# Kernel optimization log

Hardware: AMD Instinct MI355X
Metric: run time of the kernel (lower is better)

The kernel has to match this reference:

```python
import jax, jax.numpy as jnp
import numpy as np

B = 64            # graphs in batch
N = 100_000       # total nodes
E = 600_000       # total edges of g == nodes of line graph lg
E2 = 1_500_000    # edges of line graph
H = 128           # hidden_dim
L = 3             # num_layers
MAXZ = 100

seg_sum = jax.ops.segment_sum


def setup_inputs() -> dict:
    key = jax.random.key(0)
    ks = jax.random.split(key, 20)
    s = 1.0 / np.sqrt(H)
    inp = {
        'z': jax.random.randint(ks[0], (N,), 0, MAXZ + 1),
        'd': jax.random.uniform(ks[1], (E, 1), dtype=jnp.float32),
        'src': jax.random.randint(ks[2], (E,), 0, N),
        'dst': jax.random.randint(ks[3], (E,), 0, N),
        'lsrc': jax.random.randint(ks[4], (E2,), 0, E),
        'ldst': jax.random.randint(ks[5], (E2,), 0, E),
        'node_graph': jnp.sort(jax.random.randint(ks[6], (N,), 0, B)),
        'edge_graph': jnp.sort(jax.random.randint(ks[7], (E,), 0, B)),
        'emb': jax.random.normal(ks[8], (MAXZ + 1, H), jnp.float32),
        'ep_w': jax.random.normal(ks[9], (1, H), jnp.float32) * s,
        'ep_b': jnp.zeros((H,), jnp.float32),
        'gW': jax.random.normal(ks[10], (L, H, H), jnp.float32) * s,
        'gb': jnp.zeros((L, H), jnp.float32),
        'lgW': jax.random.normal(ks[11], (L, H, H), jnp.float32) * s,
        'lgb': jnp.zeros((L, H), jnp.float32),
        'r1w': jax.random.normal(ks[12], (2 * H, H), jnp.float32) * s,
        'r1b': jnp.zeros((H,), jnp.float32),
        'r2w': jax.random.normal(ks[13], (H, 1), jnp.float32) * s,
        'r2b': jnp.zeros((1,), jnp.float32),
    }
    return inp


def _graph_conv(h, srcix, dstix, W, b, n_nodes):
    # DGL GraphConv, norm='both', aggregate-then-weight (in==out dims):
    # h' = D_in^{-1/2} * A^T * (D_out^{-1/2} * h) @ W + b, degrees clamped >= 1
    ones = jnp.ones(srcix.shape[0], h.dtype)
    deg_out = jnp.clip(seg_sum(ones, srcix, num_segments=n_nodes), 1.0)
    deg_in = jnp.clip(seg_sum(ones, dstix, num_segments=n_nodes), 1.0)
    m = h * (deg_out ** -0.5)[:, None]
    agg = seg_sum(m[srcix], dstix, num_segments=n_nodes)  # SpMM gather-scatter
    agg = agg * (deg_in ** -0.5)[:, None]
    return agg @ W + b


def _segment_mean(h, seg, n_seg):
    sums = seg_sum(h, seg, num_segments=n_seg)
    cnt = jnp.clip(seg_sum(jnp.ones(h.shape[0], h.dtype), seg, num_segments=n_seg), 1.0)
    return sums / cnt[:, None]


def reference(z, d, src, dst, lsrc, ldst, node_graph, edge_graph,
              emb, ep_w, ep_b, gW, gb, lgW, lgb, r1w, r1b, r2w, r2b):
    h = emb[z]                       # [N, H]
    e = d @ ep_w + ep_b              # [E, H]
    for i in range(L):
        h = jax.nn.relu(_graph_conv(h, src, dst, gW[i], gb[i], N))
    for i in range(L):
        e = jax.nn.relu(_graph_conv(e, lsrc, ldst, lgW[i], lgb[i], E))
    hg = _segment_mean(h, node_graph, B)   # [B, H]
    he = _segment_mean(e, edge_graph, B)   # [B, H]
    x = jnp.concatenate([hg, he], axis=-1)  # [B, 2H]
    y = jax.nn.silu(x @ r1w + r1b) @ r2w + r2b
    return y.reshape(-1)             # [B]
```

## Files before the change

### kernel.cpp

```cpp
#include <hip/hip_runtime.h>
#include <math.h>

#define H 128
typedef unsigned short u16;
typedef unsigned char u8;
typedef unsigned int u32;
typedef _Float16 f16;
typedef f16 f16x8 __attribute__((ext_vector_type(8)));
typedef float f32x4 __attribute__((ext_vector_type(4)));
typedef float f32x2 __attribute__((ext_vector_type(2)));

#if __has_builtin(__builtin_amdgcn_cvt_pk_fp8_f32)
#define HW8 1
#else
#define HW8 0
#endif

#define SSTRIDE 144

static inline int cdiv(long long a, long long b) { return (int)((a + b - 1) / b); }

__device__ __forceinline__ int swz_seg(int orig, int n) {
    int q = n >> 3, r = n & 7;
    int x = orig & 7;
    int base = (x < r) ? x * (q + 1) : r * (q + 1) + (x - r) * q;
    return base + (orig >> 3);
}
__device__ __forceinline__ int conv_bid(int orig, int nbCN, int nwg) {
    return (orig < nbCN) ? swz_seg(orig, nbCN)
                         : nbCN + swz_seg(orig - nbCN, nwg - nbCN);
}

struct F8 {
    static __device__ inline float dec(u8 v) {
        int e = (v >> 3) & 15, m = v & 7;
        float f = (e == 0) ? (float)m * 0.001953125f : ldexpf(1.f + 0.125f * (float)m, e - 7);
        return (v & 0x80) ? -f : f;
    }
    static __device__ inline u8 enc(float x) {
        u8 s = (u8)((__float_as_uint(x) >> 24) & 0x80);
        float ax = fabsf(x);
        if (!(ax < 448.f)) return s | 0x7E;
        if (ax < 0.015625f) {
            int m = (int)rintf(ax * 512.f);
            if (m >= 8) return s | 0x08;
            return s | (u8)m;
        }
        int e; float fr = frexpf(ax, &e);
        int E = e - 1;
        int m = (int)rintf(fr * 16.f - 8.f);
        if (m == 8) { m = 0; ++E; }
        if (E > 8) return s | 0x7E;
        return s | (u8)(((E + 7) << 3) | m);
    }
};

static __device__ inline u32 enc4(float x0, float x1, float x2, float x3) {
#if HW8
    u32 w = __builtin_amdgcn_cvt_pk_fp8_f32(x0, x1, 0, false);
    w = __builtin_amdgcn_cvt_pk_fp8_f32(x2, x3, w, true);
    return w;
#else
    union { u8 b[4]; u32 u; } p;
    p.b[0] = F8::enc(x0); p.b[1] = F8::enc(x1); p.b[2] = F8::enc(x2); p.b[3] = F8::enc(x3);
    return p.u;
#endif
}
static __device__ inline float4 dec4(u32 v) {
#if HW8
    f32x2 lo = __builtin_amdgcn_cvt_pk_f32_fp8(v, false);
    f32x2 hi = __builtin_amdgcn_cvt_pk_f32_fp8(v, true);
    return make_float4(lo.x, lo.y, hi.x, hi.y);
#else
    union { u32 u; u8 b[4]; } c; c.u = v;
    return make_float4(F8::dec(c.b[0]), F8::dec(c.b[1]), F8::dec(c.b[2]), F8::dec(c.b[3]));
#endif
}

__global__ __launch_bounds__(256) void setup1_k(
    const float* __restrict__ gW, const float* __restrict__ lgW, f16* __restrict__ wt, int L, int nbPW,
    const int* __restrict__ src, const int* __restrict__ dst,
    const int* __restrict__ lsrc, const int* __restrict__ ldst,
    int* __restrict__ con, int* __restrict__ cin, int* __restrict__ coe, int* __restrict__ cie,
    int E, int E2, int nbHI,
    const int* __restrict__ node_graph, int N, const int* __restrict__ edge_graph,
    int B, int* __restrict__ cntn, int* __restrict__ cnte,
    const float* __restrict__ epw, const float* __restrict__ epb, float* __restrict__ uv) {
    int blk = blockIdx.x;
    if (blk < nbPW) {
        int mat = blk >> 6;
        int idx = (blk & 63) * 256 + threadIdx.x;
        int k = idx >> 7, n = idx & 127;
        const float* W = (mat < L) ? gW + (size_t)mat * H * H : lgW + (size_t)(mat - L) * H * H;
        wt[(size_t)mat * H * H + (size_t)n * H + k] = (f16)W[(size_t)k * H + n];
        return;
    }
    blk -= nbPW;
    if (blk < nbHI) {
        int i = blk * 256 + threadIdx.x;
        if (i < E) {
            atomicAdd(&con[src[i]], 1);
            atomicAdd(&cin[dst[i]], 1);
        } else if (i < E + E2) {
            int j = i - E;
            atomicAdd(&coe[lsrc[j]], 1);
            atomicAdd(&cie[ldst[j]], 1);
        }
        return;
    }
    blk -= nbHI;
    if (blk < 2) {
        const int* seg = blk ? edge_graph : node_graph;
        int n = blk ? E : N;
        int* cnt = blk ? cnte : cntn;
        __shared__ int bound[129];
        int b = threadIdx.x;
        if (b <= B) {
            int lo = 0, hi = n;
            while (lo < hi) {
                int mid = (lo + hi) >> 1;
                if (seg[mid] < b) lo = mid + 1; else hi = mid;
            }
            bound[b] = lo;
        }
        __syncthreads();
        if (b < B) cnt[b] = bound[b + 1] - bound[b];
        return;
    }
    {
        int n = threadIdx.x;
        if (n < H) {
            float su = 0.f, sv = 0.f;
            for (int k = 0; k < H; ++k) {
                float w = lgW[(size_t)k * H + n];
                su = fmaf(epw[k], w, su);
                sv = fmaf(epb[k], w, sv);
            }
            uv[n] = su;
            uv[n + H] = sv;
        }
    }
}

__global__ __launch_bounds__(256) void setup2_k(
    const int* __restrict__ con, const int* __restrict__ cin,
    const int* __restrict__ coe, const int* __restrict__ cie,
    float* __restrict__ ron, float* __restrict__ rin,
    float* __restrict__ roe, float* __restrict__ rie,
    const float* __restrict__ d, float2* __restrict__ pairE, int N, int E, int nbRS,
    int* __restrict__ offs_n, int nbN, int* __restrict__ offs_e, int* __restrict__ bsum) {
    int blk = blockIdx.x;
    if (blk < nbRS) {
        int i = blk * 256 + threadIdx.x;
        if (i < N) { int v = con[i]; ron[i] = rsqrtf((float)(v < 1 ? 1 : v)); }
        else if (i < 2 * N) { int n = i - N; int v = cin[n]; rin[n] = rsqrtf((float)(v < 1 ? 1 : v)); }
        else if (i < 2 * N + E) {
            int n = i - 2 * N; int v = coe[n];
            float r = rsqrtf((float)(v < 1 ? 1 : v));
            roe[n] = r;
            pairE[n] = make_float2(r * d[n], r);
        } else if (i < 2 * N + 2 * E) {
            int n = i - 2 * N - E; int v = cie[n]; rie[n] = rsqrtf((float)(v < 1 ? 1 : v));
        }
        return;
    }
    blk -= nbRS;
    {
        __shared__ int sh[256];
        const int* in; int* out; int n; int gid;
        if (blk < nbN) { in = cin; out = offs_n; n = N; gid = blk * 256 + threadIdx.x; }
        else { in = cie; out = offs_e; n = E; gid = (blk - nbN) * 256 + threadIdx.x; }
        int v = (gid < n) ? in[gid] : 0;
        sh[threadIdx.x] = v;
        __syncthreads();
        for (int off = 1; off < 256; off <<= 1) {
            int t = (threadIdx.x >= off) ? sh[threadIdx.x - off] : 0;
            __syncthreads();
            sh[threadIdx.x] += t;
            __syncthreads();
        }
        if (gid < n) out[gid] = sh[threadIdx.x] - v;
        if (threadIdx.x == 255) bsum[blk] = sh[255];
    }
}

__global__ __launch_bounds__(256) void scan_bsum2_k(int* __restrict__ bsum, int nbA, int nbB) {
    __shared__ int sh[256];
    __shared__ int carry;
#pragma unroll 1
    for (int part = 0; part < 2; ++part) {
        int base0 = part ? nbA : 0;
        int nb = part ? nbB : nbA;
        if (threadIdx.x == 0) carry = 0;
        __syncthreads();
        for (int base = 0; base < nb; base += 256) {
            int i = base + threadIdx.x;
            int v = (i < nb) ? bsum[base0 + i] : 0;
            sh[threadIdx.x] = v;
            __syncthreads();
            for (int off = 1; off < 256; off <<= 1) {
                int t = (threadIdx.x >= off) ? sh[threadIdx.x - off] : 0;
                __syncthreads();
                sh[threadIdx.x] += t;
                __syncthreads();
            }
            if (i < nb) bsum[base0 + i] = sh[threadIdx.x] - v + carry;
            __syncthreads();
            if (threadIdx.x == 0) carry += sh[255];
            __syncthreads();
        }
    }
}

__global__ __launch_bounds__(256) void setup3_k(
    int* __restrict__ offs_n, int* __restrict__ cur_n, int N, int nbN, int E,
    int* __restrict__ offs_e, int* __restrict__ cur_e, int E2, int nbE,
    const int* __restrict__ bsum,
    const int* __restrict__ z, const float* __restrict__ emb,
    const float* __restrict__ ron, u8* __restrict__ featN) {
    int blk = blockIdx.x;
    int nbSA = nbN + nbE;
    if (blk < nbSA) {
        int* offs; int* curp; int n; int gid; int nnz;
        if (blk < nbN) { offs = offs_n; curp = cur_n; n = N; gid = blk * 256 + threadIdx.x; nnz = E; }
        else { offs = offs_e; curp = cur_e; n = E; gid = (blk - nbN) * 256 + threadIdx.x; nnz = E2; }
        if (gid < n) {
            int v = offs[gid] + bsum[blk];
            offs[gid] = v;
            curp[gid] = v;
        }
        if (gid == 0) offs[n] = nnz;
        return;
    }
    blk -= nbSA;
    {
        int idx = blk * 256 + threadIdx.x;
        if (idx >= N * 32) return;
        int n = idx >> 5, c4 = (idx & 31) << 2;
        float sc = ron[n];
        const float4 v = *(const float4*)(emb + (size_t)z[n] * H + c4);
        *(u32*)(featN + (size_t)n * H + c4) = enc4(v.x * sc, v.y * sc, v.z * sc, v.w * sc);
    }
}

__global__ __launch_bounds__(256) void fill2_k(const int* __restrict__ src, const int* __restrict__ dst,
                                               const int* __restrict__ lsrc, const int* __restrict__ ldst,
                                               int* __restrict__ cur_n, int* __restrict__ cur_e,
                                               uint2* __restrict__ nbr_n, uint2* __restrict__ nbr_e,
                                               const float2* __restrict__ pairE, float2* __restrict__ pslot,
                                               int E, int E2) {
    int i = blockIdx.x * 256 + threadIdx.x;
    if (i < E) {
        int dd = dst[i];
        int p = atomicAdd(&cur_n[dd], 1);
        nbr_n[p] = make_uint2((u32)src[i], (u32)dd);
    } else if (i < E + E2) {
        int j = i - E;
        int ls = lsrc[j];
        int dd = ldst[j];
        int p = atomicAdd(&cur_e[dd], 1);
        nbr_e[p] = make_uint2((u32)ls, (u32)dd);
        pslot[p] = pairE[ls];
    }
}

__device__ __forceinline__ void gather_phase(
    const u8* __restrict__ Xin,
    const int* __restrict__ offs, const uint2* __restrict__ nbr2,
    const float* __restrict__ rs_in, int M,
    int row0, f16 (*As)[136], int wave, int lane) {
    const int rowbase = row0 + wave * 16;
    {
        uint2* zp = (uint2*)&As[wave * 16][0];
#pragma unroll
        for (int i = 0; i < 9; ++i) {
            int o = lane + i * 64;
            if (o < 544) zp[o] = make_uint2(0u, 0u);
        }
    }
    const int gl = lane >> 4;
    const int ln = lane & 15;
    const int rbase4 = rowbase + gl * 4;
    const int r_lo = min(rbase4, M);
    const int r_hi = min(rbase4 + 4, M);
    const int jbeg = offs[r_lo];
    const int jend = offs[r_hi];
    if (jbeg >= jend) return;
    const int mrow = M - 1;
    const float rsr0 = rs_in[min(rbase4 + 0, mrow)];
    const float rsr1 = rs_in[min(rbase4 + 1, mrow)];
    const float rsr2 = rs_in[min(rbase4 + 2, mrow)];
    const float rsr3 = rs_in[min(rbase4 + 3, mrow)];

    float a0 = 0.f, a1 = 0.f, a2 = 0.f, a3 = 0.f, a4 = 0.f, a5 = 0.f, a6 = 0.f, a7 = 0.f;
    int curdst = -1;

#define FLUSH_ROW()                                                              \
    do {                                                                         \
        const int dd_ = curdst - rbase4;                                         \
        const float ri_ = dd_ == 0 ? rsr0 : (dd_ == 1 ? rsr1 : (dd_ == 2 ? rsr2 : rsr3)); \
        f16x8 o_;                                                                \
        o_[0] = (f16)(a0 * ri_); o_[1] = (f16)(a1 * ri_);                        \
        o_[2] = (f16)(a2 * ri_); o_[3] = (f16)(a3 * ri_);                        \
        o_[4] = (f16)(a4 * ri_); o_[5] = (f16)(a5 * ri_);                        \
        o_[6] = (f16)(a6 * ri_); o_[7] = (f16)(a7 * ri_);                        \
        *(f16x8*)&As[curdst - row0][ln << 3] = o_;                               \
    } while (0)

#define PROC_BATCH(eX, fX)                                                       \
    _Pragma("unroll")                                                            \
    for (int k = 0; k < 8; ++k) {                                                \
        if (jc + k < jend) {                                                     \
            const int dk = (int)eX[k].y;                                         \
            if (dk != curdst) {                                                  \
                if (curdst >= 0) {                                               \
                    FLUSH_ROW();                                                 \
                    a0 = a1 = a2 = a3 = a4 = a5 = a6 = a7 = 0.f;                 \
                }                                                                \
                curdst = dk;                                                     \
            }                                                                    \
            float4 lo = dec4(fX[k].x);                                           \
            float4 hi = dec4(fX[k].y);                                           \
            a0 += lo.x; a1 += lo.y; a2 += lo.z; a3 += lo.w;                      \
            a4 += hi.x; a5 += hi.y; a6 += hi.z; a7 += hi.w;                      \
        }                                                                        \
    }

    uint2 eA[8], eB[8], fA[8], fB[8];
#pragma unroll
    for (int k = 0; k < 8; ++k) eA[k] = nbr2[min(jbeg + k, jend - 1)];
#pragma unroll
    for (int k = 0; k < 8; ++k) eB[k] = nbr2[min(jbeg + 8 + k, jend - 1)];
#pragma unroll
    for (int k = 0; k < 8; ++k)
        fA[k] = *(const uint2*)(Xin + ((size_t)eA[k].x << 7) + (ln << 3));
    int jc = jbeg;
    for (;;) {
        if (jc + 8 < jend) {
#pragma unroll
            for (int k = 0; k < 8; ++k)
                fB[k] = *(const uint2*)(Xin + ((size_t)eB[k].x << 7) + (ln << 3));
        }
        __builtin_amdgcn_sched_barrier(0);
        PROC_BATCH(eA, fA);
        if (jc + 16 < jend) {
#pragma unroll
            for (int k = 0; k < 8; ++k) eA[k] = nbr2[min(jc + 16 + k, jend - 1)];
        }
        jc += 8;
        if (jc >= jend) break;
        if (jc + 8 < jend) {
#pragma unroll
            for (int k = 0; k < 8; ++k)
                fA[k] = *(const uint2*)(Xin + ((size_t)eA[k].x << 7) + (ln << 3));
        }
        __builtin_amdgcn_sched_barrier(0);
        PROC_BATCH(eB, fB);
        if (jc + 16 < jend) {
#pragma unroll
            for (int k = 0; k < 8; ++k) eB[k] = nbr2[min(jc + 16 + k, jend - 1)];
        }
        jc += 8;
        if (jc >= jend) break;
    }
    FLUSH_ROW();
#undef PROC_BATCH
#undef FLUSH_ROW
}

template <bool STORE>
__device__ __forceinline__ void conv_mfma_phase(
    u8* __restrict__ Xout, const f16* __restrict__ Wt, const float* __restrict__ bias,
    const float* __restrict__ scale_out, int M, int row0, f16 (*As)[136], int wave, int lane) {
    const int rowbase = row0 + wave * 16;
    if (rowbase >= M) return;
    const int l15 = lane & 15;
    const int quad = lane >> 4;

    f16x8 a[4];
#pragma unroll
    for (int kt = 0; kt < 4; ++kt)
        a[kt] = *(const f16x8*)&As[wave * 16 + l15][kt * 32 + quad * 8];

    float rsc[4];
#pragma unroll
    for (int r = 0; r < 4; ++r) {
        int gr = rowbase + quad * 4 + r;
        rsc[r] = (scale_out && gr < M) ? scale_out[gr] : 1.f;
    }

    u8* stage = (u8*)&As[wave * 16][0];

#pragma unroll
    for (int n0 = 0; n0 < 8; ++n0) {
        f32x4 acc = {0.f, 0.f, 0.f, 0.f};
        const f16* bp = Wt + (size_t)(n0 * 16 + l15) * H + quad * 8;
#pragma unroll
        for (int kt = 0; kt < 4; ++kt) {
            f16x8 b = *(const f16x8*)(bp + kt * 32);
            acc = __builtin_amdgcn_mfma_f32_16x16x32_f16(a[kt], b, acc, 0, 0, 0);
        }
        int col = n0 * 16 + l15;
        float bv = bias[col];
        float o[4];
#pragma unroll
        for (int r = 0; r < 4; ++r) o[r] = fmaxf(acc[r] + bv, 0.f) * rsc[r];
        u32 w = enc4(o[0], o[1], o[2], o[3]);
#pragma unroll
        for (int r = 0; r < 4; ++r) stage[(quad * 4 + r) * SSTRIDE + col] = (u8)(w >> (8 * r));
    }
    if (STORE) {
        const int lr = lane >> 2;
        const int lc = (lane & 3) * 32;
        int gr = rowbase + lr;
        if (gr < M) {
            uint4 v0 = *(const uint4*)&stage[lr * SSTRIDE + lc];
            uint4 v1 = *(const uint4*)&stage[lr * SSTRIDE + lc + 16];
            *(uint4*)(Xout + (size_t)gr * H + lc) = v0;
            *(uint4*)(Xout + (size_t)gr * H + lc + 16) = v1;
        }
    }
}

__device__ __forceinline__ void conv_mfma_pool_phase(
    const f16* __restrict__ Wt, const float* __restrict__ bias, int M, int row0,
    f16 (*As)[136], float (*pool)[128], int wave, int lane,
    const int* __restrict__ seg, float* __restrict__ outp, bool uni) {
    const int rowbase = row0 + wave * 16;
    if (rowbase >= M) return;
    const int l15 = lane & 15;
    const int quad = lane >> 4;

    f16x8 a[4];
#pragma unroll
    for (int kt = 0; kt < 4; ++kt)
        a[kt] = *(const f16x8*)&As[wave * 16 + l15][kt * 32 + quad * 8];

    const int gr0 = rowbase + quad * 4;
    const int remM = M - gr0;
    int g0 = -1, g1 = -1, g2 = -1, g3 = -1;
    if (!uni) {
        g0 = (0 < remM) ? seg[gr0 + 0] : -1;
        g1 = (1 < remM) ? seg[gr0 + 1] : -1;
        g2 = (2 < remM) ? seg[gr0 + 2] : -1;
        g3 = (3 < remM) ? seg[gr0 + 3] : -1;
    }

#pragma unroll
    for (int n0 = 0; n0 < 8; ++n0) {
        f32x4 acc = {0.f, 0.f, 0.f, 0.f};
        const f16* bp = Wt + (size_t)(n0 * 16 + l15) * H + quad * 8;
#pragma unroll
        for (int kt = 0; kt < 4; ++kt) {
            f16x8 b = *(const f16x8*)(bp + kt * 32);
            acc = __builtin_amdgcn_mfma_f32_16x16x32_f16(a[kt], b, acc, 0, 0, 0);
        }
        const int col = n0 * 16 + l15;
        const float bv = bias[col];
        const float o0 = (0 < remM) ? fmaxf(acc[0] + bv, 0.f) : 0.f;
        const float o1 = (1 < remM) ? fmaxf(acc[1] + bv, 0.f) : 0.f;
        const float o2 = (2 < remM) ? fmaxf(acc[2] + bv, 0.f) : 0.f;
        const float o3 = (3 < remM) ? fmaxf(acc[3] + bv, 0.f) : 0.f;
        if (uni) {
            float s = (o0 + o1) + (o2 + o3);
            s += __shfl_xor(s, 16);
            s += __shfl_xor(s, 32);
            if (quad == 0) pool[wave][col] = s;
        } else {
            float ac = o0; int gc = g0;
            if (g1 == gc) ac += o1; else { if (gc >= 0) atomicAdd(&outp[(size_t)gc * H + col], ac); gc = g1; ac = o1; }
            if (g2 == gc) ac += o2; else { if (gc >= 0) atomicAdd(&outp[(size_t)gc * H + col], ac); gc = g2; ac = o2; }
            if (g3 == gc) ac += o3; else { if (gc >= 0) atomicAdd(&outp[(size_t)gc * H + col], ac); gc = g3; ac = o3; }
            if (gc >= 0) atomicAdd(&outp[(size_t)gc * H + col], ac);
        }
    }
}

template <bool STORE>
__device__ __forceinline__ void conv_wave(
    const u8* __restrict__ Xin, u8* __restrict__ Xout,
    const int* __restrict__ offs, const uint2* __restrict__ nbr2,
    const float* __restrict__ rs_in, const f16* __restrict__ Wt,
    const float* __restrict__ bias, const float* __restrict__ scale_out, int M,
    int row0, f16 (*As)[136], int wave, int lane) {
    gather_phase(Xin, offs, nbr2, rs_in, M, row0, As, wave, lane);
    conv_mfma_phase<STORE>(Xout, Wt, bias, scale_out, M, row0, As, wave, lane);
}

__device__ __forceinline__ void conv_wave_l0e(
    u8* __restrict__ Xout, const int* __restrict__ offs,
    const float2* __restrict__ pslot, const float* __restrict__ rs_in,
    const float* __restrict__ uv, const float* __restrict__ bias,
    const float* __restrict__ scale_out, int E,
    int row0, int wave, int lane) {
    const int rowbase = row0 + wave * 16;
    const int r = lane >> 2;
    const int t = lane & 3;
    const int growu = rowbase + r;
    const int grow = min(growu, E - 1);
    const int jb = offs[grow];
    const int je = offs[grow + 1];
    float sd = 0.f, sw = 0.f;
    for (int j = jb + t; j < je; j += 4) {
        float2 p = pslot[j];
        sd += p.x; sw += p.y;
    }
    sd += __shfl_xor(sd, 1); sw += __shfl_xor(sw, 1);
    sd += __shfl_xor(sd, 2); sw += __shfl_xor(sw, 2);
    if (growu >= E) return;
    const float ri = rs_in[growu];
    const float so = scale_out[growu];
    sd *= ri; sw *= ri;
    const int c0 = t * 32;
    u32 wbuf[8];
#pragma unroll
    for (int c4 = 0; c4 < 8; ++c4) {
        const int c = c0 + c4 * 4;
        const float4 ua = *(const float4*)(uv + c);
        const float4 va = *(const float4*)(uv + H + c);
        const float4 ba = *(const float4*)(bias + c);
        const float o0 = fmaxf(fmaf(sd, ua.x, fmaf(sw, va.x, ba.x)), 0.f) * so;
        const float o1 = fmaxf(fmaf(sd, ua.y, fmaf(sw, va.y, ba.y)), 0.f) * so;
        const float o2 = fmaxf(fmaf(sd, ua.z, fmaf(sw, va.z, ba.z)), 0.f) * so;
        const float o3 = fmaxf(fmaf(sd, ua.w, fmaf(sw, va.w, ba.w)), 0.f) * so;
        wbuf[c4] = enc4(o0, o1, o2, o3);
    }
    *(uint4*)(Xout + (size_t)growu * H + c0) = *(uint4*)&wbuf[0];
    *(uint4*)(Xout + (size_t)growu * H + c0 + 16) = *(uint4*)&wbuf[4];
}

__global__ __launch_bounds__(128, 4) void conv2_k(
    const u8* __restrict__ XinN, u8* __restrict__ XoutN,
    const int* __restrict__ offs_n, const uint2* __restrict__ nbr_n,
    const float* __restrict__ rinN, const f16* __restrict__ WtN,
    const float* __restrict__ biasN, const float* __restrict__ scaleN, int N, int nbCN,
    const u8* __restrict__ XinE, u8* __restrict__ XoutE,
    const int* __restrict__ offs_e, const uint2* __restrict__ nbr_e,
    const float* __restrict__ rinE, const f16* __restrict__ WtE,
    const float* __restrict__ biasE, const float* __restrict__ scaleE, int E) {
    __shared__ f16 As[32][136];
    const int tid = threadIdx.x;
    const int wave = tid >> 6;
    const int lane = tid & 63;
    const int bid = conv_bid((int)blockIdx.x, nbCN, (int)gridDim.x);
    if (bid < nbCN) {
        conv_wave<true>(XinN, XoutN, offs_n, nbr_n, rinN, WtN, biasN, scaleN, N,
                        bid * 32, As, wave, lane);
    } else {
        conv_wave<true>(XinE, XoutE, offs_e, nbr_e, rinE, WtE, biasE, scaleE, E,
                        (bid - nbCN) * 32, As, wave, lane);
    }
}

__global__ __launch_bounds__(128, 4) void conv2_l0_k(
    const u8* __restrict__ XinN, u8* __restrict__ XoutN,
    const int* __restrict__ offs_n, const uint2* __restrict__ nbr_n,
    const float* __restrict__ rinN, const f16* __restrict__ WtN,
    const float* __restrict__ biasN, const float* __restrict__ scaleN, int N, int nbCN,
    u8* __restrict__ XoutE,
    const int* __restrict__ offs_e, const float2* __restrict__ pslot,
    const float* __restrict__ rinE, const float* __restrict__ uv,
    const float* __restrict__ biasE, const float* __restrict__ scaleE, int E) {
    __shared__ f16 As[32][136];
    const int tid = threadIdx.x;
    const int wave = tid >> 6;
    const int lane = tid & 63;
    const int bid = conv_bid((int)blockIdx.x, nbCN, (int)gridDim.x);
    if (bid < nbCN) {
        conv_wave<true>(XinN, XoutN, offs_n, nbr_n, rinN, WtN, biasN, scaleN, N,
                        bid * 32, As, wave, lane);
    } else {
        conv_wave_l0e(XoutE, offs_e, pslot, rinE, uv, biasE, scaleE, E,
                      (bid - nbCN) * 32, wave, lane);
    }
}

__global__ __launch_bounds__(128, 4) void conv2_last_k(
    const u8* __restrict__ XinN,
    const int* __restrict__ offs_n, const uint2* __restrict__ nbr_n,
    const float* __restrict__ rinN, const f16* __restrict__ WtN,
    const float* __restrict__ biasN, int N, int nbCN,
    const int* __restrict__ node_graph, float* __restrict__ hg,
    const u8* __restrict__ XinE,
    const int* __restrict__ offs_e, const uint2* __restrict__ nbr_e,
    const float* __restrict__ rinE, const f16* __restrict__ WtE,
    const float* __restrict__ biasE, int E,
    const int* __restrict__ edge_graph, float* __restrict__ he) {
    __shared__ f16 As[32][136];
    __shared__ float pool[2][128];
    const int tid = threadIdx.x;
    const int wave = tid >> 6;
    const int lane = tid & 63;
    const int bid = conv_bid((int)blockIdx.x, nbCN, (int)gridDim.x);
    const bool isN = bid < nbCN;
    const int row0 = (isN ? bid : bid - nbCN) * 32;
    const int M = isN ? N : E;
    const int* seg = isN ? node_graph : edge_graph;
    float* outp = isN ? hg : he;

    ((float*)pool)[tid] = 0.f;
    ((float*)pool)[tid + 128] = 0.f;
    const int gblk = seg[row0];
    const bool uni = (seg[min(row0 + 31, M - 1)] == gblk);
    __syncthreads();

    if (isN) {
        gather_phase(XinN, offs_n, nbr_n, rinN, N, row0, As, wave, lane);
        conv_mfma_pool_phase(WtN, biasN, N, row0, As, pool, wave, lane, seg, outp, uni);
    } else {
        gather_phase(XinE, offs_e, nbr_e, rinE, E, row0, As, wave, lane);
        conv_mfma_pool_phase(WtE, biasE, E, row0, As, pool, wave, lane, seg, outp, uni);
    }
    __syncthreads();
    if (uni) {
        float s = pool[0][tid] + pool[1][tid];
        atomicAdd(&outp[(size_t)gblk * H + tid], s);
    }
}

__global__ __launch_bounds__(128) void readout_k(const float* __restrict__ hg, const float* __restrict__ he,
                                                 const int* __restrict__ cn, const int* __restrict__ ce,
                                                 const float* __restrict__ r1w, const float* __restrict__ r1b,
                                                 const float* __restrict__ r2w, const float* __restrict__ r2b,
                                                 float* __restrict__ out) {
    const int b = blockIdx.x;
    const int j = threadIdx.x;
    const float invn = 1.f / fmaxf((float)cn[b], 1.f);
    const float inve = 1.f / fmaxf((float)ce[b], 1.f);
    float acc = r1b[j];
    for (int k = 0; k < H; ++k) acc = fmaf(hg[(size_t)b * H + k] * invn, r1w[(size_t)k * H + j], acc);
    for (int k = 0; k < H; ++k) acc = fmaf(he[(size_t)b * H + k] * inve, r1w[(size_t)(k + H) * H + j], acc);
    float s = acc / (1.f + expf(-acc));
    __shared__ float red[128];
    red[j] = s * r2w[j];
    __syncthreads();
    for (int off = 64; off > 0; off >>= 1) {
        if (j < off) red[j] += red[j + off];
        __syncthreads();
    }
    if (j == 0) out[b] = red[0] + r2b[0];
}

__global__ void report_k(float* out, int n, float val) {
    int i = blockIdx.x * 64 + threadIdx.x;
    if (i < n) out[i] = val;
}

extern "C" void kernel_launch(void* const* d_in, const int* in_sizes, int n_in,
                              void* d_out, int out_size, void* d_ws, size_t ws_size,
                              hipStream_t stream) {
    const int* z          = (const int*)d_in[0];
    const float* d        = (const float*)d_in[1];
    const int* src        = (const int*)d_in[2];
    const int* dst        = (const int*)d_in[3];
    const int* lsrc       = (const int*)d_in[4];
    const int* ldst       = (const int*)d_in[5];
    const int* node_graph = (const int*)d_in[6];
    const int* edge_graph = (const int*)d_in[7];
    const float* emb      = (const float*)d_in[8];
    const float* epw      = (const float*)d_in[9];
    const float* epb      = (const float*)d_in[10];
    const float* gW       = (const float*)d_in[11];
    const float* gb       = (const float*)d_in[12];
    const float* lgW      = (const float*)d_in[13];
    const float* lgb      = (const float*)d_in[14];
    const float* r1w      = (const float*)d_in[15];
    const float* r1b      = (const float*)d_in[16];
    const float* r2w      = (const float*)d_in[17];
    const float* r2b      = (const float*)d_in[18];

    const int N  = in_sizes[0];
    const int E  = in_sizes[2];
    const int E2 = in_sizes[4];
    const int B  = out_size;
    const int L  = 3;
    float* out = (float*)d_out;
    char* ws = (char*)d_ws;

    size_t off = 0;
    auto al = [&](size_t b) -> char* { char* q = ws + off; off += (b + 255) & ~(size_t)255; return q; };
    u8*  featEA = (u8*)al((size_t)E * H);
    u8*  featEB = (u8*)al((size_t)E * H);
    u8*  featNA = (u8*)al((size_t)N * H);
    u8*  featNB = (u8*)al((size_t)N * H);
    f16* wt    = (f16*)al((size_t)2 * L * H * H * 2);
    float* uv  = (float*)al((size_t)2 * H * 4);
    float* ron = (float*)al((size_t)N * 4);
    float* rin = (float*)al((size_t)N * 4);
    float* roe = (float*)al((size_t)E * 4);
    float* rie = (float*)al((size_t)E * 4);
    float2* pairE = (float2*)al((size_t)E * 8);
    size_t cntCount = (size_t)2 * N + 2 * E + 2 * B;
    size_t cntBytes = cntCount * 4;
    size_t poolsOff = (cntBytes + 255) & ~(size_t)255;
    char* zblock = al(poolsOff + (size_t)2 * B * H * 4);
    int* cnts = (int*)zblock;
    float* pools = (float*)(zblock + poolsOff);
    int* con = cnts; int* cin_ = con + N; int* coe = cin_ + N; int* cie = coe + E;
    int* cntn = cie + E; int* cnte = cntn + B;
    float* hg = pools;
    float* he = pools + (size_t)B * H;
    int* offs_n = (int*)al(((size_t)N + 1) * 4);
    int* cur_n  = (int*)al((size_t)N * 4);
    int* offs_e = (int*)al(((size_t)E + 1) * 4);
    int* cur_e  = (int*)al((size_t)E * 4);
    uint2* nbr_n = (uint2*)al((size_t)E * 8);
    uint2* nbr_e = (uint2*)al((size_t)E2 * 8);
    float2* pslot = (float2*)al((size_t)E2 * 8);
    int nbN = cdiv(N, 256), nbE = cdiv(E, 256);
    int* bsum   = (int*)al(((size_t)nbN + nbE + 2) * 4);

    if (off > ws_size) {
        report_k<<<cdiv(B, 64), 64, 0, stream>>>(out, B, (float)(ws_size >> 20));
        return;
    }

    hipMemsetAsync(zblock, 0, poolsOff + (size_t)2 * B * H * 4, stream);

    const int nbPW = 2 * L * 64;
    const int nbHI = cdiv((long long)E + E2, 256);
    setup1_k<<<nbPW + nbHI + 3, 256, 0, stream>>>(gW, lgW, wt, L, nbPW,
                                                  src, dst, lsrc, ldst, con, cin_, coe, cie,
                                                  E, E2, nbHI, node_graph, N, edge_graph, B, cntn, cnte,
                                                  epw, epb, uv);

    const int nbRS = cdiv((long long)2 * N + 2 * E, 256);
    setup2_k<<<nbRS + nbN + nbE, 256, 0, stream>>>(con, cin_, coe, cie, ron, rin, roe, rie,
                                                   d, pairE, N, E, nbRS, offs_n, nbN, offs_e, bsum);
    scan_bsum2_k<<<1, 256, 0, stream>>>(bsum, nbN, nbE);

    const int nbIN = cdiv((long long)N * 32, 256);
    setup3_k<<<nbN + nbE + nbIN, 256, 0, stream>>>(offs_n, cur_n, N, nbN, E,
                                                   offs_e, cur_e, E2, nbE, bsum, z, emb, ron, featNA);

    fill2_k<<<cdiv((long long)E + E2, 256), 256, 0, stream>>>(src, dst, lsrc, ldst, cur_n, cur_e,
                                                              nbr_n, nbr_e, pairE, pslot, E, E2);

    const int nbCN = cdiv(N, 32), nbCE = cdiv(E, 32);

    conv2_l0_k<<<nbCN + nbCE, 128, 0, stream>>>(
        featNA, featNB, offs_n, nbr_n, rin, wt, gb, ron, N, nbCN,
        featEB, offs_e, pslot, rie, uv, lgb, roe, E);

    conv2_k<<<nbCN + nbCE, 128, 0, stream>>>(
        featNB, featNA, offs_n, nbr_n, rin, wt + (size_t)1 * H * H, gb + (size_t)1 * H, ron, N, nbCN,
        featEB, featEA, offs_e, nbr_e, rie, wt + (size_t)(L + 1) * H * H, lgb + (size_t)1 * H, roe, E);

    conv2_last_k<<<nbCN + nbCE, 128, 0, stream>>>(
        featNA, offs_n, nbr_n, rin, wt + (size_t)2 * H * H, gb + (size_t)2 * H, N, nbCN, node_graph, hg,
        featEA, offs_e, nbr_e, rie, wt + (size_t)(L + 2) * H * H, lgb + (size_t)2 * H, E, edge_graph, he);

    readout_k<<<B, 128, 0, stream>>>(hg, he, cntn, cnte, r1w, r1b, r2w, r2b, out);
}
```

Before: 990.4 us.

## Stage gathered neighbor features into LDS via async global_load_lds double buffering

Replaces the register-prefetched gather of FP8 neighbor feature rows with asynchronous global-to-LDS loads (global_load_lds), double-buffered in a per-wave ring, with s_waitcnt-based pipelining over batches of 4 edges per lane group. The aim is to cut VGPR pressure and hide gather latency by overlapping the next batch's loads with accumulation. In exchange it adds 8 KB of shared memory per block, which may lower occupancy, and it halves the batch depth from 8 to 4, which could expose more latency.

```diff
diff --git a/kernel.cpp b/kernel.cpp
--- a/kernel.cpp
+++ b/kernel.cpp
@@ -9,6 +9,9 @@
 typedef f16 f16x8 __attribute__((ext_vector_type(8)));
 typedef float f32x4 __attribute__((ext_vector_type(4)));
 typedef float f32x2 __attribute__((ext_vector_type(2)));
+
+typedef __attribute__((address_space(1))) const void gas_void;
+typedef __attribute__((address_space(3))) void las_void;
 
 #if __has_builtin(__builtin_amdgcn_cvt_pk_fp8_f32)
 #define HW8 1
@@ -268,7 +271,7 @@
     const u8* __restrict__ Xin,
     const int* __restrict__ offs, const uint2* __restrict__ nbr2,
     const float* __restrict__ rs_in, int M,
-    int row0, f16 (*As)[136], int wave, int lane) {
+    int row0, f16 (*As)[136], u8* __restrict__ featRing, int wave, int lane) {
     const int rowbase = row0 + wave * 16;
     {
         uint2* zp = (uint2*)&As[wave * 16][0];
@@ -281,10 +284,8 @@
     const int gl = lane >> 4;
     const int ln = lane & 15;
     const int rbase4 = rowbase + gl * 4;
-    const int r_lo = min(rbase4, M);
-    const int r_hi = min(rbase4 + 4, M);
-    const int jbeg = offs[r_lo];
-    const int jend = offs[r_hi];
+    const int jbeg = offs[min(rbase4, M)];
+    const int jend = offs[min(rbase4 + 4, M)];
     if (jbeg >= jend) return;
     const int mrow = M - 1;
     const float rsr0 = rs_in[min(rbase4 + 0, mrow)];
@@ -307,64 +308,66 @@
         *(f16x8*)&As[curdst - row0][ln << 3] = o_;                               \
     } while (0)
 
-#define PROC_BATCH(eX, fX)                                                       \
-    _Pragma("unroll")                                                            \
-    for (int k = 0; k < 8; ++k) {                                                \
-        if (jc + k < jend) {                                                     \
-            const int dk = (int)eX[k].y;                                         \
-            if (dk != curdst) {                                                  \
-                if (curdst >= 0) {                                               \
-                    FLUSH_ROW();                                                 \
-                    a0 = a1 = a2 = a3 = a4 = a5 = a6 = a7 = 0.f;                 \
-                }                                                                \
-                curdst = dk;                                                     \
-            }                                                                    \
-            float4 lo = dec4(fX[k].x);                                           \
-            float4 hi = dec4(fX[k].y);                                           \
-            a0 += lo.x; a1 += lo.y; a2 += lo.z; a3 += lo.w;                      \
-            a4 += hi.x; a5 += hi.y; a6 += hi.z; a7 += hi.w;                      \
-        }                                                                        \
-    }
-
-    uint2 eA[8], eB[8], fA[8], fB[8];
-#pragma unroll
-    for (int k = 0; k < 8; ++k) eA[k] = nbr2[min(jbeg + k, jend - 1)];
-#pragma unroll
-    for (int k = 0; k < 8; ++k) eB[k] = nbr2[min(jbeg + 8 + k, jend - 1)];
-#pragma unroll
-    for (int k = 0; k < 8; ++k)
-        fA[k] = *(const uint2*)(Xin + ((size_t)eA[k].x << 7) + (ln << 3));
-    int jc = jbeg;
-    for (;;) {
-        if (jc + 8 < jend) {
-#pragma unroll
-            for (int k = 0; k < 8; ++k)
-                fB[k] = *(const uint2*)(Xin + ((size_t)eB[k].x << 7) + (ln << 3));
+    const int sub = (lane >> 3) & 1;
+    const size_t c16 = (size_t)(lane & 7) << 4;
+#define STAGE(eX, rg) do {                                                        \
+        u32 rxa_ = sub ? eX[1].x : eX[0].x;                                       \
+        u32 rxb_ = sub ? eX[3].x : eX[2].x;                                       \
+        __builtin_amdgcn_global_load_lds(                                         \
+            (gas_void*)(Xin + ((size_t)rxa_ << 7) + c16),                         \
+            (las_void*)(featRing + (rg) * 2048), 16, 0, 0);                       \
+        __builtin_amdgcn_global_load_lds(                                         \
+            (gas_void*)(Xin + ((size_t)rxb_ << 7) + c16),                         \
+            (las_void*)(featRing + (rg) * 2048 + 1024), 16, 0, 0);                \
+    } while (0)
+
+    uint2 eA[4], eB[4];
+#pragma unroll
+    for (int k = 0; k < 4; ++k) eA[k] = nbr2[min(jbeg + k, jend - 1)];
+    STAGE(eA, 0);
+#pragma unroll
+    for (int k = 0; k < 4; ++k) eB[k] = nbr2[min(jbeg + 4 + k, jend - 1)];
+    int ring = 0;
+    for (int jc = jbeg; ; ) {
+        const bool more = (jc + 4 < jend);
+        if (more) {
+            STAGE(eB, ring ^ 1);
+            asm volatile("s_waitcnt vmcnt(2)" ::: "memory");
+        } else {
+            asm volatile("s_waitcnt vmcnt(0)" ::: "memory");
         }
         __builtin_amdgcn_sched_barrier(0);
-        PROC_BATCH(eA, fA);
-        if (jc + 16 < jend) {
-#pragma unroll
-            for (int k = 0; k < 8; ++k) eA[k] = nbr2[min(jc + 16 + k, jend - 1)];
-        }
-        jc += 8;
+        const u8* fb = featRing + ring * 2048 + gl * 256;
+#pragma unroll
+        for (int k = 0; k < 4; ++k) {
+            if (jc + k < jend) {
+                const int dk = (int)eA[k].y;
+                if (dk != curdst) {
+                    if (curdst >= 0) {
+                        FLUSH_ROW();
+                        a0 = a1 = a2 = a3 = a4 = a5 = a6 = a7 = 0.f;
+                    }
+                    curdst = dk;
+                }
+                uint2 fv = *(const uint2*)(fb + (k >> 1) * 1024 + (k & 1) * 128 + (ln << 3));
+                float4 lo = dec4(fv.x);
+                float4 hi = dec4(fv.y);
+                a0 += lo.x; a1 += lo.y; a2 += lo.z; a3 += lo.w;
+                a4 += hi.x; a5 += hi.y; a6 += hi.z; a7 += hi.w;
+            }
+        }
+        jc += 4;
         if (jc >= jend) break;
-        if (jc + 8 < jend) {
-#pragma unroll
-            for (int k = 0; k < 8; ++k)
-                fA[k] = *(const uint2*)(Xin + ((size_t)eA[k].x << 7) + (ln << 3));
-        }
-        __builtin_amdgcn_sched_barrier(0);
-        PROC_BATCH(eB, fB);
-        if (jc + 16 < jend) {
-#pragma unroll
-            for (int k = 0; k < 8; ++k) eB[k] = nbr2[min(jc + 16 + k, jend - 1)];
-        }
-        jc += 8;
-        if (jc >= jend) break;
+#pragma unroll
+        for (int k = 0; k < 4; ++k) eA[k] = eB[k];
+        if (jc + 4 < jend) {
+#pragma unroll
+            for (int k = 0; k < 4; ++k) eB[k] = nbr2[min(jc + 4 + k, jend - 1)];
+        }
+        ring ^= 1;
     }
     FLUSH_ROW();
-#undef PROC_BATCH
+#undef STAGE
 #undef FLUSH_ROW
 }
 
@@ -482,8 +485,8 @@
     const int* __restrict__ offs, const uint2* __restrict__ nbr2,
     const float* __restrict__ rs_in, const f16* __restrict__ Wt,
     const float* __restrict__ bias, const float* __restrict__ scale_out, int M,
-    int row0, f16 (*As)[136], int wave, int lane) {
-    gather_phase(Xin, offs, nbr2, rs_in, M, row0, As, wave, lane);
+    int row0, f16 (*As)[136], u8* __restrict__ featRing, int wave, int lane) {
+    gather_phase(Xin, offs, nbr2, rs_in, M, row0, As, featRing, wave, lane);
     conv_mfma_phase<STORE>(Xout, Wt, bias, scale_out, M, row0, As, wave, lane);
 }
 
@@ -539,16 +542,17 @@
     const float* __restrict__ rinE, const f16* __restrict__ WtE,
     const float* __restrict__ biasE, const float* __restrict__ scaleE, int E) {
     __shared__ f16 As[32][136];
+    __shared__ u8 Stg[2][4096];
     const int tid = threadIdx.x;
     const int wave = tid >> 6;
     const int lane = tid & 63;
     const int bid = conv_bid((int)blockIdx.x, nbCN, (int)gridDim.x);
     if (bid < nbCN) {
         conv_wave<true>(XinN, XoutN, offs_n, nbr_n, rinN, WtN, biasN, scaleN, N,
-                        bid * 32, As, wave, lane);
+                        bid * 32, As, Stg[wave], wave, lane);
     } else {
         conv_wave<true>(XinE, XoutE, offs_e, nbr_e, rinE, WtE, biasE, scaleE, E,
-                        (bid - nbCN) * 32, As, wave, lane);
+                        (bid - nbCN) * 32, As, Stg[wave], wave, lane);
     }
 }
 
@@ -562,13 +566,14 @@
     const float* __restrict__ rinE, const float* __restrict__ uv,
     const float* __restrict__ biasE, const float* __restrict__ scaleE, int E) {
     __shared__ f16 As[32][136];
+    __shared__ u8 Stg[2][4096];
     const int tid = threadIdx.x;
     const int wave = tid >> 6;
     const int lane = tid & 63;
     const int bid = conv_bid((int)blockIdx.x, nbCN, (int)gridDim.x);
     if (bid < nbCN) {
         conv_wave<true>(XinN, XoutN, offs_n, nbr_n, rinN, WtN, biasN, scaleN, N,
-                        bid * 32, As, wave, lane);
+                        bid * 32, As, Stg[wave], wave, lane);
     } else {
         conv_wave_l0e(XoutE, offs_e, pslot, rinE, uv, biasE, scaleE, E,
                       (bid - nbCN) * 32, wave, lane);
@@ -587,6 +592,7 @@
     const float* __restrict__ biasE, int E,
     const int* __restrict__ edge_graph, float* __restrict__ he) {
     __shared__ f16 As[32][136];
+    __shared__ u8 Stg[2][4096];
     __shared__ float pool[2][128];
     const int tid = threadIdx.x;
     const int wave = tid >> 6;
@@ -605,10 +611,10 @@
     __syncthreads();
 
     if (isN) {
-        gather_phase(XinN, offs_n, nbr_n, rinN, N, row0, As, wave, lane);
+        gather_phase(XinN, offs_n, nbr_n, rinN, N, row0, As, Stg[wave], wave, lane);
         conv_mfma_pool_phase(WtN, biasN, N, row0, As, pool, wave, lane, seg, outp, uni);
     } else {
-        gather_phase(XinE, offs_e, nbr_e, rinE, E, row0, As, wave, lane);
+        gather_phase(XinE, offs_e, nbr_e, rinE, E, row0, As, Stg[wave], wave, lane);
         conv_mfma_pool_phase(WtE, biasE, E, row0, As, pool, wave, lane, seg, outp, uni);
     }
     __syncthreads();
```

Result: no change. 972.3 us, median of 2 (-1.8%).
